# Optimization experiments

Hardware: AMD Instinct MI355X
Metric: run time of the kernel (lower is better)

The kernel has to match this reference:

```python
import jax, jax.numpy as jnp
import numpy as np

HEADS = 16

def _split_qkv(qkv, h):
    # faithful to rearrange 'b t (d k h) -> k b h t d' with k=3
    b, t, e3 = qkv.shape
    d = e3 // (3 * h)
    qkv = qkv.reshape(b, t, d, 3, h)          # (b,t,d,k,h), d-major packing
    qkv = jnp.transpose(qkv, (3, 0, 4, 1, 2))  # (k,b,h,t,d)
    return qkv[0], qkv[1], qkv[2]

def setup_inputs() -> dict:
    key = jax.random.key(0)
    ks = jax.random.split(key, 5)
    b, t, e = 2, 2048, 1024
    s = e ** -0.5
    return {
        "x": jax.random.normal(ks[0], (b, t, e), jnp.float32),
        "tx": jax.random.normal(ks[1], (b, t, e), jnp.float32),
        "Wqkv": jax.random.normal(ks[2], (3 * e, e), jnp.float32) * s,
        "Wtqkv": jax.random.normal(ks[3], (3 * e, e), jnp.float32) * s,
        "Wout": jax.random.normal(ks[4], (e, e), jnp.float32) * s,
    }

def reference(x, tx, Wqkv, Wtqkv, Wout):
    h = HEADS
    e = x.shape[-1]
    d_head = e // h
    scale = jnp.float32(d_head ** 0.5)  # NOTE: module MULTIPLIES by sqrt(d_head)

    qkv = x @ Wqkv.T     # (b,t,3e)
    tqkv = tx @ Wtqkv.T  # (b,t,3e)
    _q, k, v = _split_qkv(qkv, h)      # each (b,h,t,d)
    tq, _tk, _tv = _split_qkv(tqkv, h)

    energy = jnp.einsum('bhid,bhjd->bhij', tq, k) * scale  # (b,h,t,t)
    attn = jax.nn.softmax(energy, axis=-1)
    out = jnp.einsum('bhij,bhjd->bhid', attn, v)           # (b,h,t,d)
    b, _, t, d = out.shape
    out = jnp.transpose(out, (0, 2, 1, 3)).reshape(b, t, h * d)  # 'b h t d -> b t (h d)'
    return out @ Wout.T
```

## Files before the change

### kernel.cpp

```cpp
#include <hip/hip_runtime.h>

typedef unsigned short u16;
typedef unsigned int u32;
typedef __attribute__((ext_vector_type(8))) short short8;
typedef __attribute__((ext_vector_type(4))) float f32x4;

__device__ inline u16 f32_to_bf16(float f) {
  u32 u = __float_as_uint(f);
  u += 0x7fffu + ((u >> 16) & 1u);
  return (u16)(u >> 16);
}
__device__ inline float bf16_to_f32(u16 s) {
  return __uint_as_float(((u32)s) << 16);
}

#if __has_builtin(__builtin_amdgcn_exp2f)
#define EXP2F(x) __builtin_amdgcn_exp2f(x)
#else
#define EXP2F(x) exp2f(x)
#endif

__device__ inline void dma16(const void* gp, void* lp) {
  __builtin_amdgcn_global_load_lds(
      (const __attribute__((address_space(1))) u32*)gp,
      (__attribute__((address_space(3))) u32*)lp, 16, 0, 0);
}

__device__ inline u32 pack_hi16(u32 a, u32 b) {
  return __builtin_amdgcn_perm(b, a, 0x07060302u);
}
__device__ inline uint4 pack_bf16_8(const uint4 a, const uint4 b) {
  uint4 r;
  r.x = pack_hi16(a.x, a.y);
  r.y = pack_hi16(a.z, a.w);
  r.z = pack_hi16(b.x, b.y);
  r.w = pack_hi16(b.z, b.w);
  return r;
}
__device__ inline void split8(const uint4 a, const uint4 b, uint4& hi, uint4& lo) {
  u32 u[8] = {a.x, a.y, a.z, a.w, b.x, b.y, b.z, b.w};
  u32 l[8];
#pragma unroll
  for (int j = 0; j < 8; ++j)
    l[j] = __float_as_uint(__uint_as_float(u[j]) - __uint_as_float(u[j] & 0xffff0000u));
  hi.x = pack_hi16(u[0], u[1]); hi.y = pack_hi16(u[2], u[3]);
  hi.z = pack_hi16(u[4], u[5]); hi.w = pack_hi16(u[6], u[7]);
  lo.x = pack_hi16(l[0], l[1]); lo.y = pack_hi16(l[2], l[3]);
  lo.z = pack_hi16(l[4], l[5]); lo.w = pack_hi16(l[6], l[7]);
}

__global__ void repack_w(const float* __restrict__ Wqkv, const float* __restrict__ Wtqkv,
                         const float* __restrict__ Wout,
                         u16* __restrict__ Wtq_hi, u16* __restrict__ Wtq_lo,
                         u16* __restrict__ Wk_hi,  u16* __restrict__ Wk_lo,
                         u16* __restrict__ Wv_hi,  u16* __restrict__ Woutb) {
  int r = blockIdx.x;
  int part = r >> 10;
  int rr = r & 1023;
  int h = rr >> 6, d = rr & 63;
  const float* src;
  u16 *dh, *dl = nullptr;
  if (part == 0)      { src = Wtqkv + (size_t)(d * 48 + h) * 1024;      dh = Wtq_hi + (size_t)rr * 1024; dl = Wtq_lo + (size_t)rr * 1024; }
  else if (part == 1) { src = Wqkv  + (size_t)(d * 48 + 16 + h) * 1024; dh = Wk_hi  + (size_t)rr * 1024; dl = Wk_lo  + (size_t)rr * 1024; }
  else if (part == 2) { src = Wqkv  + (size_t)(d * 48 + 32 + h) * 1024; dh = Wv_hi  + (size_t)rr * 1024; }
  else                { src = Wout  + (size_t)rr * 1024;                dh = Woutb  + (size_t)rr * 1024; }
  int c = threadIdx.x * 4;
  f32x4 v = *(const f32x4*)&src[c];
  u32 hv[4], lv[4];
#pragma unroll
  for (int j = 0; j < 4; ++j) {
    u16 hb = f32_to_bf16(v[j]);
    hv[j] = hb;
    lv[j] = f32_to_bf16(v[j] - bf16_to_f32(hb));
  }
  uint2 ho; ho.x = hv[0] | (hv[1] << 16); ho.y = hv[2] | (hv[3] << 16);
  *(uint2*)&dh[c] = ho;
  if (dl) {
    uint2 lo; lo.x = lv[0] | (lv[1] << 16); lo.y = lv[2] | (lv[3] << 16);
    *(uint2*)&dl[c] = lo;
  }
}

__global__ __launch_bounds__(256) __attribute__((amdgpu_waves_per_eu(2)))
void proj_fused(const float* __restrict__ x, const float* __restrict__ tx,
                const u16* __restrict__ Wtq_hi, const u16* __restrict__ Wtq_lo,
                const u16* __restrict__ Wk_hi,  const u16* __restrict__ Wk_lo,
                const u16* __restrict__ Wv_hi,
                u16* __restrict__ Qhi, u16* __restrict__ Qlo,
                u16* __restrict__ Khi, u16* __restrict__ Klo,
                u16* __restrict__ Vt, float qscale) {
  __shared__ __align__(16) float Fs[2][128][32];
  __shared__ __align__(16) u16   Hs[2][128][32];
  __shared__ __align__(16) u16   Ls[2][128][32];
  const int tid = threadIdx.x;
  const int wid = tid >> 6, lane = tid & 63;
  const int g = lane >> 4, l16 = lane & 15;
  const int job = blockIdx.y;
  const int tile = blockIdx.x;
  const int wm = (wid & 1) * 64, wn = (wid >> 1) * 64;

  int m0, n0, N, frow0, hrow0;
  const float* Fsrc;
  const u16 *Hsrc;
  const u16 *Lsrc = nullptr;
  if (job == 0) {
    m0 = (tile >> 3) * 128; n0 = (tile & 7) * 128; N = 1024;
    Fsrc = tx; frow0 = m0; Hsrc = Wtq_hi; Lsrc = Wtq_lo; hrow0 = n0;
  } else if (job == 1) {
    m0 = (tile >> 3) * 128; n0 = (tile & 7) * 128; N = 1024;
    Fsrc = x; frow0 = m0; Hsrc = Wk_hi; Lsrc = Wk_lo; hrow0 = n0;
  } else {
    m0 = (tile >> 5) * 128; n0 = (tile & 31) * 128; N = 4096;
    Fsrc = x; frow0 = n0; Hsrc = Wv_hi; hrow0 = m0;
  }

  const int lrow8 = lane >> 3;
  const int gf = (lane & 7) ^ lrow8;
  const int lrow4 = lane >> 2;
  const int gh = (lane & 3) ^ ((lrow4 ^ (lrow4 >> 2)) & 3);

  auto issue_chunk = [&](int k0, int p) {
#pragma unroll
    for (int t = 0; t < 4; ++t) {
      int rb = wid * 32 + t * 8;
      dma16(&Fsrc[(size_t)(frow0 + rb + lrow8) * 1024 + k0 + gf * 4], &Fs[p][rb][0]);
    }
#pragma unroll
    for (int t = 0; t < 2; ++t) {
      int rb = wid * 32 + t * 16;
      size_t ro = (size_t)(hrow0 + rb + lrow4) * 1024 + k0 + gh * 8;
      dma16(&Hsrc[ro], &Hs[p][rb][0]);
      if (job != 2) dma16(&Lsrc[ro], &Ls[p][rb][0]);
    }
  };

  f32x4 acc[4][4];
  const f32x4 zero4 = {0.f, 0.f, 0.f, 0.f};
#pragma unroll
  for (int i = 0; i < 4; ++i)
#pragma unroll
    for (int j = 0; j < 4; ++j) acc[i][j] = zero4;

  const int sw8 = l16 & 7;
  const int sw4 = (l16 ^ (l16 >> 2)) & 3;

  issue_chunk(0, 0);

  for (int k0 = 0; k0 < 1024; k0 += 32) {
    const int p = (k0 >> 5) & 1;
    __syncthreads();
    if (k0 + 32 < 1024) issue_chunk(k0 + 32, p ^ 1);

    if (job != 2) {
      short8 ah[4], al[4], bh4[4], bl4[4];
#pragma unroll
      for (int mi = 0; mi < 4; ++mi) {
        const int R = wm + mi * 16 + l16;
        uint4 u0 = *(const uint4*)&Fs[p][R][((2 * g) ^ sw8) * 4];
        uint4 u1 = *(const uint4*)&Fs[p][R][((2 * g + 1) ^ sw8) * 4];
        uint4 hi, lo;
        split8(u0, u1, hi, lo);
        ah[mi] = *(short8*)&hi;
        al[mi] = *(short8*)&lo;
      }
#pragma unroll
      for (int ni = 0; ni < 4; ++ni) {
        const int R = wn + ni * 16 + l16;
        const int col = (g ^ sw4) * 8;
        bh4[ni] = *(const short8*)&Hs[p][R][col];
        bl4[ni] = *(const short8*)&Ls[p][R][col];
      }
#pragma unroll
      for (int mi = 0; mi < 4; ++mi)
#pragma unroll
        for (int ni = 0; ni < 4; ++ni) {
          acc[mi][ni] = __builtin_amdgcn_mfma_f32_16x16x32_bf16(ah[mi], bh4[ni], acc[mi][ni], 0, 0, 0);
          acc[mi][ni] = __builtin_amdgcn_mfma_f32_16x16x32_bf16(ah[mi], bl4[ni], acc[mi][ni], 0, 0, 0);
          acc[mi][ni] = __builtin_amdgcn_mfma_f32_16x16x32_bf16(al[mi], bh4[ni], acc[mi][ni], 0, 0, 0);
        }
    } else {
      short8 av[4], bx[4];
#pragma unroll
      for (int mi = 0; mi < 4; ++mi)
        av[mi] = *(const short8*)&Hs[p][wm + mi * 16 + l16][(g ^ sw4) * 8];
#pragma unroll
      for (int ni = 0; ni < 4; ++ni) {
        const int R = wn + ni * 16 + l16;
        uint4 u0 = *(const uint4*)&Fs[p][R][((2 * g) ^ sw8) * 4];
        uint4 u1 = *(const uint4*)&Fs[p][R][((2 * g + 1) ^ sw8) * 4];
        uint4 t = pack_bf16_8(u0, u1);
        bx[ni] = *(short8*)&t;
      }
#pragma unroll
      for (int mi = 0; mi < 4; ++mi)
#pragma unroll
        for (int ni = 0; ni < 4; ++ni)
          acc[mi][ni] = __builtin_amdgcn_mfma_f32_16x16x32_bf16(av[mi], bx[ni], acc[mi][ni], 0, 0, 0);
    }
  }

  u16* Chi = (job == 0) ? Qhi : ((job == 1) ? Khi : Vt);
  u16* Clo = (job == 0) ? Qlo : Klo;
  float scale = (job == 0) ? qscale : 1.0f;
#pragma unroll
  for (int mi = 0; mi < 4; ++mi)
#pragma unroll
    for (int ni = 0; ni < 4; ++ni) {
      int row = m0 + wm + mi * 16 + g * 4;
      int col = n0 + wn + ni * 16 + l16;
#pragma unroll
      for (int r = 0; r < 4; ++r) {
        float v = acc[mi][ni][r] * scale;
        size_t o = (size_t)(row + r) * N + col;
        u32 uv = __float_as_uint(v);
        if (job != 2) {
          Chi[o] = (u16)(uv >> 16);
          float lo = v - __uint_as_float(uv & 0xffff0000u);
          Clo[o] = (u16)(__float_as_uint(lo) >> 16);
        } else {
          Chi[o] = (u16)(uv >> 16);
        }
      }
    }
}

__global__ __launch_bounds__(256) __attribute__((amdgpu_waves_per_eu(2, 4)))
void gemm_out(const u16* __restrict__ A, const u16* __restrict__ B,
              float* __restrict__ C, int M, int N, int K) {
  __shared__ __align__(16) u16 As[128][40];
  __shared__ __align__(16) u16 Bs[64][40];
  const int tid = threadIdx.x;
  const int wid = tid >> 6, lane = tid & 63;
  const int g = lane >> 4, l16 = lane & 15;
  const int m0 = blockIdx.y * 128, n0 = blockIdx.x * 64;
  const int wm = (wid & 1) * 64, wn = (wid >> 1) * 32;

  f32x4 acc[4][2];
  const f32x4 zero4 = {0.f, 0.f, 0.f, 0.f};
#pragma unroll
  for (int i = 0; i < 4; ++i)
#pragma unroll
    for (int j = 0; j < 2; ++j) acc[i][j] = zero4;

  uint4 pa[2], pb;
  const int rowA0 = tid >> 2, colA = (tid & 3) * 8;
  const int rowA1 = rowA0 + 64;
  const int rowB = tid >> 2, colB = (tid & 3) * 8;
  pa[0] = *(const uint4*)&A[(size_t)(m0 + rowA0) * K + colA];
  pa[1] = *(const uint4*)&A[(size_t)(m0 + rowA1) * K + colA];
  pb    = *(const uint4*)&B[(size_t)(n0 + rowB) * K + colB];

  for (int k0 = 0; k0 < K; k0 += 32) {
    __syncthreads();
    *(uint4*)&As[rowA0][colA] = pa[0];
    *(uint4*)&As[rowA1][colA] = pa[1];
    *(uint4*)&Bs[rowB][colB] = pb;
    __syncthreads();
    if (k0 + 32 < K) {
      pa[0] = *(const uint4*)&A[(size_t)(m0 + rowA0) * K + k0 + 32 + colA];
      pa[1] = *(const uint4*)&A[(size_t)(m0 + rowA1) * K + k0 + 32 + colA];
      pb    = *(const uint4*)&B[(size_t)(n0 + rowB) * K + k0 + 32 + colB];
    }
    short8 af[4], bfr[2];
#pragma unroll
    for (int mi = 0; mi < 4; ++mi)
      af[mi] = *(const short8*)&As[wm + mi * 16 + l16][g * 8];
#pragma unroll
    for (int ni = 0; ni < 2; ++ni)
      bfr[ni] = *(const short8*)&Bs[wn + ni * 16 + l16][g * 8];
#pragma unroll
    for (int mi = 0; mi < 4; ++mi)
#pragma unroll
      for (int ni = 0; ni < 2; ++ni)
        acc[mi][ni] = __builtin_amdgcn_mfma_f32_16x16x32_bf16(af[mi], bfr[ni], acc[mi][ni], 0, 0, 0);
  }
#pragma unroll
  for (int mi = 0; mi < 4; ++mi)
#pragma unroll
    for (int ni = 0; ni < 2; ++ni) {
      int row = m0 + wm + mi * 16 + g * 4;
      int col = n0 + wn + ni * 16 + l16;
#pragma unroll
      for (int r = 0; r < 4; ++r)
        C[(size_t)(row + r) * N + col] = acc[mi][ni][r];
    }
}

__global__ __launch_bounds__(256)
void attn_fwd(const u16* __restrict__ Qhi, const u16* __restrict__ Qlo,
              const u16* __restrict__ Khi, const u16* __restrict__ Klo,
              const u16* __restrict__ Vt, u16* __restrict__ O) {
  const int blk = blockIdx.x;
  const int qb = blk & 15, bh = blk >> 4;
  const int h = bh & 15, b = bh >> 4;
  const int t0 = qb * 128;
  const int tid = threadIdx.x, wid = tid >> 6, lane = tid & 63;
  const int g = lane >> 4, l16 = lane & 15;
  const int par = g & 1;
  const int hi2 = g >> 1;

  __shared__ __align__(16) u16 Ksh[2][64][64];
  __shared__ __align__(16) u16 Ksl[2][64][64];
  __shared__ __align__(16) u16 Vs[2][64][64];

  const int lrow = lane >> 3;
  const int lgc  = (lane & 7) ^ lrow;
  const size_t kbase = (size_t)(b * 2048) * 1024 + h * 64;
  const size_t vbase = (size_t)(h * 64) * 4096 + b * 2048;

  auto issue_chunk = [&](int j0, int p) {
#pragma unroll
    for (int t = 0; t < 2; ++t) {
      int rbase = wid * 16 + t * 8;
      int row = rbase + lrow;
      dma16(&Khi[kbase + (size_t)(j0 + row) * 1024 + lgc * 8], &Ksh[p][rbase][0]);
      dma16(&Klo[kbase + (size_t)(j0 + row) * 1024 + lgc * 8], &Ksl[p][rbase][0]);
      dma16(&Vt[vbase + (size_t)row * 4096 + j0 + lgc * 8],    &Vs[p][rbase][0]);
    }
  };

  short8 qh[2][2], ql[2][2];
#pragma unroll
  for (int mt = 0; mt < 2; ++mt)
#pragma unroll
    for (int ks = 0; ks < 2; ++ks) {
      size_t qo = (size_t)(b * 2048 + t0 + wid * 32 + mt * 16 + l16) * 1024
                  + h * 64 + ks * 32 + g * 8;
      qh[mt][ks] = *(const short8*)&Qhi[qo];
      ql[mt][ks] = *(const short8*)&Qlo[qo];
    }

  float mrow[2] = {-1.0e30f, -1.0e30f};
  const f32x4 zero4 = {0.f, 0.f, 0.f, 0.f};
  f32x4 acc[2][5];
#pragma unroll
  for (int mt = 0; mt < 2; ++mt)
#pragma unroll
    for (int dn = 0; dn < 5; ++dn) acc[mt][dn] = zero4;

  short8 ones8;
#pragma unroll
  for (int j = 0; j < 8; ++j) ones8[j] = (short)0x3f80;

  union PB { u32 w[4]; short8 v; };

  issue_chunk(0, 0);

  for (int i = 0; i < 32; ++i) {
    const int p = i & 1;
    __syncthreads();
    if (i < 31) issue_chunk((i + 1) * 64, 1 - p);

    f32x4 s[2][4];
#pragma unroll
    for (int mt = 0; mt < 2; ++mt)
#pragma unroll
      for (int n = 0; n < 4; ++n) s[mt][n] = zero4;
#pragma unroll
    for (int ks = 0; ks < 2; ++ks)
#pragma unroll
      for (int n = 0; n < 4; ++n) {
        int col = (((ks * 4 + g) ^ (l16 & 7))) * 8;
        short8 kh = *(const short8*)&Ksh[p][n * 16 + l16][col];
        short8 kl = *(const short8*)&Ksl[p][n * 16 + l16][col];
        s[0][n] = __builtin_amdgcn_mfma_f32_16x16x32_bf16(kh, qh[0][ks], s[0][n], 0, 0, 0);
        s[1][n] = __builtin_amdgcn_mfma_f32_16x16x32_bf16(kh, qh[1][ks], s[1][n], 0, 0, 0);
        s[0][n] = __builtin_amdgcn_mfma_f32_16x16x32_bf16(kh, ql[0][ks], s[0][n], 0, 0, 0);
        s[1][n] = __builtin_amdgcn_mfma_f32_16x16x32_bf16(kh, ql[1][ks], s[1][n], 0, 0, 0);
        s[0][n] = __builtin_amdgcn_mfma_f32_16x16x32_bf16(kl, qh[0][ks], s[0][n], 0, 0, 0);
        s[1][n] = __builtin_amdgcn_mfma_f32_16x16x32_bf16(kl, qh[1][ks], s[1][n], 0, 0, 0);
      }

    PB pb[2][2];
#pragma unroll
    for (int mt = 0; mt < 2; ++mt) {
      float cm = -1.0e30f;
#pragma unroll
      for (int n = 0; n < 4; ++n)
#pragma unroll
        for (int r = 0; r < 4; ++r) cm = fmaxf(cm, s[mt][n][r]);
      cm = fmaxf(cm, __shfl_xor(cm, 16));
      cm = fmaxf(cm, __shfl_xor(cm, 32));
      float mnew = fmaxf(mrow[mt], cm);
      float al = EXP2F(mrow[mt] - mnew);
      mrow[mt] = mnew;
#pragma unroll
      for (int dn = 0; dn < 5; ++dn)
#pragma unroll
        for (int r = 0; r < 4; ++r) acc[mt][dn][r] *= al;

      u32 pk[4][2];
#pragma unroll
      for (int n = 0; n < 4; ++n) {
        float p0 = EXP2F(s[mt][n][0] - mnew);
        float p1 = EXP2F(s[mt][n][1] - mnew);
        float p2 = EXP2F(s[mt][n][2] - mnew);
        float p3 = EXP2F(s[mt][n][3] - mnew);
        pk[n][0] = pack_hi16(__float_as_uint(p0), __float_as_uint(p1));
        pk[n][1] = pack_hi16(__float_as_uint(p2), __float_as_uint(p3));
      }
#pragma unroll
      for (int ks2 = 0; ks2 < 2; ++ks2)
#pragma unroll
        for (int t = 0; t < 4; ++t) {
          int src = (((par << 1) | (t >> 1)) << 4) | l16;
          u32 w0 = (u32)__shfl((int)pk[2 * ks2][t & 1], src);
          u32 w1 = (u32)__shfl((int)pk[2 * ks2 + 1][t & 1], src);
          pb[mt][ks2].w[t] = hi2 ? w1 : w0;
        }
    }

#pragma unroll
    for (int ks2 = 0; ks2 < 2; ++ks2) {
#pragma unroll
      for (int dn = 0; dn < 4; ++dn) {
        int col = (((ks2 * 4 + g) ^ (l16 & 7))) * 8;
        short8 vb = *(const short8*)&Vs[p][dn * 16 + l16][col];
        acc[0][dn] = __builtin_amdgcn_mfma_f32_16x16x32_bf16(vb, pb[0][ks2].v, acc[0][dn], 0, 0, 0);
        acc[1][dn] = __builtin_amdgcn_mfma_f32_16x16x32_bf16(vb, pb[1][ks2].v, acc[1][dn], 0, 0, 0);
      }
      acc[0][4] = __builtin_amdgcn_mfma_f32_16x16x32_bf16(ones8, pb[0][ks2].v, acc[0][4], 0, 0, 0);
      acc[1][4] = __builtin_amdgcn_mfma_f32_16x16x32_bf16(ones8, pb[1][ks2].v, acc[1][4], 0, 0, 0);
    }
  }

#pragma unroll
  for (int mt = 0; mt < 2; ++mt) {
    float inv = 1.f / acc[mt][4][0];
    int qrow = t0 + wid * 32 + mt * 16 + l16;
    size_t base = (size_t)(b * 2048 + qrow) * 1024 + h * 64;
#pragma unroll
    for (int dn = 0; dn < 4; ++dn) {
      u32 o0 = pack_hi16(__float_as_uint(acc[mt][dn][0] * inv),
                         __float_as_uint(acc[mt][dn][1] * inv));
      u32 o1 = pack_hi16(__float_as_uint(acc[mt][dn][2] * inv),
                         __float_as_uint(acc[mt][dn][3] * inv));
      uint2 ov; ov.x = o0; ov.y = o1;
      *(uint2*)&O[base + dn * 16 + g * 4] = ov;
    }
  }
}

extern "C" void kernel_launch(void* const* d_in, const int* in_sizes, int n_in,
                              void* d_out, int out_size, void* d_ws, size_t ws_size,
                              hipStream_t stream) {
  const float* x     = (const float*)d_in[0];
  const float* tx    = (const float*)d_in[1];
  const float* Wqkv  = (const float*)d_in[2];
  const float* Wtqkv = (const float*)d_in[3];
  const float* Wout  = (const float*)d_in[4];
  float* out = (float*)d_out;

  char* ws = (char*)d_ws;
  const size_t MB = 1048576;
  u16* Wtq_hi = (u16*)(ws + 0 * MB);
  u16* Wtq_lo = (u16*)(ws + 2 * MB);
  u16* Wk_hi  = (u16*)(ws + 4 * MB);
  u16* Wk_lo  = (u16*)(ws + 6 * MB);
  u16* Wv_hi  = (u16*)(ws + 8 * MB);
  u16* Woutb  = (u16*)(ws + 10 * MB);
  u16* Qhi    = (u16*)(ws + 12 * MB);
  u16* Qlo    = (u16*)(ws + 20 * MB);
  u16* Khi    = (u16*)(ws + 28 * MB);
  u16* Klo    = (u16*)(ws + 36 * MB);
  u16* Vt     = (u16*)(ws + 44 * MB);
  u16* Ob     = (u16*)(ws + 0 * MB);
  if (ws_size < 52 * MB) return;

  const float QSCALE = 8.0f * 1.4426950408889634f;

  repack_w<<<4096, 256, 0, stream>>>(Wqkv, Wtqkv, Wout,
                                     Wtq_hi, Wtq_lo, Wk_hi, Wk_lo, Wv_hi, Woutb);
  proj_fused<<<dim3(256, 3), 256, 0, stream>>>(x, tx, Wtq_hi, Wtq_lo, Wk_hi, Wk_lo,
                                               Wv_hi, Qhi, Qlo, Khi, Klo, Vt, QSCALE);
  attn_fwd<<<512, 256, 0, stream>>>(Qhi, Qlo, Khi, Klo, Vt, Ob);
  gemm_out<<<dim3(16, 32), 256, 0, stream>>>(Ob, Woutb, out, 4096, 1024, 1024);
}
```

Measured before the change: 316.8 us.

## Use 8 waves per attention block and skip rescaling when max grows little

```diff
diff --git a/kernel.cpp b/kernel.cpp
--- a/kernel.cpp
+++ b/kernel.cpp
@@ -286,7 +286,7 @@
     }
 }
 
-__global__ __launch_bounds__(256)
+__global__ __launch_bounds__(512)
 void attn_fwd(const u16* __restrict__ Qhi, const u16* __restrict__ Qlo,
               const u16* __restrict__ Khi, const u16* __restrict__ Klo,
               const u16* __restrict__ Vt, u16* __restrict__ O) {
@@ -309,34 +309,26 @@
   const size_t vbase = (size_t)(h * 64) * 4096 + b * 2048;
 
   auto issue_chunk = [&](int j0, int p) {
-#pragma unroll
-    for (int t = 0; t < 2; ++t) {
-      int rbase = wid * 16 + t * 8;
-      int row = rbase + lrow;
-      dma16(&Khi[kbase + (size_t)(j0 + row) * 1024 + lgc * 8], &Ksh[p][rbase][0]);
-      dma16(&Klo[kbase + (size_t)(j0 + row) * 1024 + lgc * 8], &Ksl[p][rbase][0]);
-      dma16(&Vt[vbase + (size_t)row * 4096 + j0 + lgc * 8],    &Vs[p][rbase][0]);
-    }
+    const int row = wid * 8 + lrow;
+    dma16(&Khi[kbase + (size_t)(j0 + row) * 1024 + lgc * 8], &Ksh[p][wid * 8][0]);
+    dma16(&Klo[kbase + (size_t)(j0 + row) * 1024 + lgc * 8], &Ksl[p][wid * 8][0]);
+    dma16(&Vt[vbase + (size_t)row * 4096 + j0 + lgc * 8],    &Vs[p][wid * 8][0]);
   };
 
-  short8 qh[2][2], ql[2][2];
-#pragma unroll
-  for (int mt = 0; mt < 2; ++mt)
-#pragma unroll
-    for (int ks = 0; ks < 2; ++ks) {
-      size_t qo = (size_t)(b * 2048 + t0 + wid * 32 + mt * 16 + l16) * 1024
-                  + h * 64 + ks * 32 + g * 8;
-      qh[mt][ks] = *(const short8*)&Qhi[qo];
-      ql[mt][ks] = *(const short8*)&Qlo[qo];
-    }
-
-  float mrow[2] = {-1.0e30f, -1.0e30f};
+  short8 qh[2], ql[2];
+#pragma unroll
+  for (int ks = 0; ks < 2; ++ks) {
+    size_t qo = (size_t)(b * 2048 + t0 + wid * 16 + l16) * 1024
+                + h * 64 + ks * 32 + g * 8;
+    qh[ks] = *(const short8*)&Qhi[qo];
+    ql[ks] = *(const short8*)&Qlo[qo];
+  }
+
+  float mrow = -1.0e30f;
   const f32x4 zero4 = {0.f, 0.f, 0.f, 0.f};
-  f32x4 acc[2][5];
-#pragma unroll
-  for (int mt = 0; mt < 2; ++mt)
-#pragma unroll
-    for (int dn = 0; dn < 5; ++dn) acc[mt][dn] = zero4;
+  f32x4 acc[5];
+#pragma unroll
+  for (int dn = 0; dn < 5; ++dn) acc[dn] = zero4;
 
   short8 ones8;
 #pragma unroll
@@ -351,11 +343,9 @@
     __syncthreads();
     if (i < 31) issue_chunk((i + 1) * 64, 1 - p);
 
-    f32x4 s[2][4];
-#pragma unroll
-    for (int mt = 0; mt < 2; ++mt)
-#pragma unroll
-      for (int n = 0; n < 4; ++n) s[mt][n] = zero4;
+    f32x4 s[4];
+#pragma unroll
+    for (int n = 0; n < 4; ++n) s[n] = zero4;
 #pragma unroll
     for (int ks = 0; ks < 2; ++ks)
 #pragma unroll
@@ -363,52 +353,48 @@
         int col = (((ks * 4 + g) ^ (l16 & 7))) * 8;
         short8 kh = *(const short8*)&Ksh[p][n * 16 + l16][col];
         short8 kl = *(const short8*)&Ksl[p][n * 16 + l16][col];
-        s[0][n] = __builtin_amdgcn_mfma_f32_16x16x32_bf16(kh, qh[0][ks], s[0][n], 0, 0, 0);
-        s[1][n] = __builtin_amdgcn_mfma_f32_16x16x32_bf16(kh, qh[1][ks], s[1][n], 0, 0, 0);
-        s[0][n] = __builtin_amdgcn_mfma_f32_16x16x32_bf16(kh, ql[0][ks], s[0][n], 0, 0, 0);
-        s[1][n] = __builtin_amdgcn_mfma_f32_16x16x32_bf16(kh, ql[1][ks], s[1][n], 0, 0, 0);
-        s[0][n] = __builtin_amdgcn_mfma_f32_16x16x32_bf16(kl, qh[0][ks], s[0][n], 0, 0, 0);
-        s[1][n] = __builtin_amdgcn_mfma_f32_16x16x32_bf16(kl, qh[1][ks], s[1][n], 0, 0, 0);
-      }
-
-    PB pb[2][2];
-#pragma unroll
-    for (int mt = 0; mt < 2; ++mt) {
-      float cm = -1.0e30f;
-#pragma unroll
-      for (int n = 0; n < 4; ++n)
-#pragma unroll
-        for (int r = 0; r < 4; ++r) cm = fmaxf(cm, s[mt][n][r]);
-      cm = fmaxf(cm, __shfl_xor(cm, 16));
-      cm = fmaxf(cm, __shfl_xor(cm, 32));
-      float mnew = fmaxf(mrow[mt], cm);
-      float al = EXP2F(mrow[mt] - mnew);
-      mrow[mt] = mnew;
+        s[n] = __builtin_amdgcn_mfma_f32_16x16x32_bf16(kh, qh[ks], s[n], 0, 0, 0);
+        s[n] = __builtin_amdgcn_mfma_f32_16x16x32_bf16(kh, ql[ks], s[n], 0, 0, 0);
+        s[n] = __builtin_amdgcn_mfma_f32_16x16x32_bf16(kl, qh[ks], s[n], 0, 0, 0);
+      }
+
+    float cm = -1.0e30f;
+#pragma unroll
+    for (int n = 0; n < 4; ++n)
+#pragma unroll
+      for (int r = 0; r < 4; ++r) cm = fmaxf(cm, s[n][r]);
+    cm = fmaxf(cm, __shfl_xor(cm, 16));
+    cm = fmaxf(cm, __shfl_xor(cm, 32));
+    if (!__all(cm <= mrow + 8.0f)) {
+      float mnew = fmaxf(mrow, cm);
+      float al = EXP2F(mrow - mnew);
+      mrow = mnew;
 #pragma unroll
       for (int dn = 0; dn < 5; ++dn)
 #pragma unroll
-        for (int r = 0; r < 4; ++r) acc[mt][dn][r] *= al;
-
-      u32 pk[4][2];
-#pragma unroll
-      for (int n = 0; n < 4; ++n) {
-        float p0 = EXP2F(s[mt][n][0] - mnew);
-        float p1 = EXP2F(s[mt][n][1] - mnew);
-        float p2 = EXP2F(s[mt][n][2] - mnew);
-        float p3 = EXP2F(s[mt][n][3] - mnew);
-        pk[n][0] = pack_hi16(__float_as_uint(p0), __float_as_uint(p1));
-        pk[n][1] = pack_hi16(__float_as_uint(p2), __float_as_uint(p3));
-      }
-#pragma unroll
-      for (int ks2 = 0; ks2 < 2; ++ks2)
-#pragma unroll
-        for (int t = 0; t < 4; ++t) {
-          int src = (((par << 1) | (t >> 1)) << 4) | l16;
-          u32 w0 = (u32)__shfl((int)pk[2 * ks2][t & 1], src);
-          u32 w1 = (u32)__shfl((int)pk[2 * ks2 + 1][t & 1], src);
-          pb[mt][ks2].w[t] = hi2 ? w1 : w0;
-        }
-    }
+        for (int r = 0; r < 4; ++r) acc[dn][r] *= al;
+    }
+
+    u32 pk[4][2];
+#pragma unroll
+    for (int n = 0; n < 4; ++n) {
+      float p0 = EXP2F(s[n][0] - mrow);
+      float p1 = EXP2F(s[n][1] - mrow);
+      float p2 = EXP2F(s[n][2] - mrow);
+      float p3 = EXP2F(s[n][3] - mrow);
+      pk[n][0] = pack_hi16(__float_as_uint(p0), __float_as_uint(p1));
+      pk[n][1] = pack_hi16(__float_as_uint(p2), __float_as_uint(p3));
+    }
+    PB pb[2];
+#pragma unroll
+    for (int ks2 = 0; ks2 < 2; ++ks2)
+#pragma unroll
+      for (int t = 0; t < 4; ++t) {
+        int src = (((par << 1) | (t >> 1)) << 4) | l16;
+        u32 w0 = (u32)__shfl((int)pk[2 * ks2][t & 1], src);
+        u32 w1 = (u32)__shfl((int)pk[2 * ks2 + 1][t & 1], src);
+        pb[ks2].w[t] = hi2 ? w1 : w0;
+      }
 
 #pragma unroll
     for (int ks2 = 0; ks2 < 2; ++ks2) {
@@ -416,28 +402,23 @@
       for (int dn = 0; dn < 4; ++dn) {
         int col = (((ks2 * 4 + g) ^ (l16 & 7))) * 8;
         short8 vb = *(const short8*)&Vs[p][dn * 16 + l16][col];
-        acc[0][dn] = __builtin_amdgcn_mfma_f32_16x16x32_bf16(vb, pb[0][ks2].v, acc[0][dn], 0, 0, 0);
-        acc[1][dn] = __builtin_amdgcn_mfma_f32_16x16x32_bf16(vb, pb[1][ks2].v, acc[1][dn], 0, 0, 0);
-      }
-      acc[0][4] = __builtin_amdgcn_mfma_f32_16x16x32_bf16(ones8, pb[0][ks2].v, acc[0][4], 0, 0, 0);
-      acc[1][4] = __builtin_amdgcn_mfma_f32_16x16x32_bf16(ones8, pb[1][ks2].v, acc[1][4], 0, 0, 0);
-    }
-  }
-
-#pragma unroll
-  for (int mt = 0; mt < 2; ++mt) {
-    float inv = 1.f / acc[mt][4][0];
-    int qrow = t0 + wid * 32 + mt * 16 + l16;
-    size_t base = (size_t)(b * 2048 + qrow) * 1024 + h * 64;
-#pragma unroll
-    for (int dn = 0; dn < 4; ++dn) {
-      u32 o0 = pack_hi16(__float_as_uint(acc[mt][dn][0] * inv),
-                         __float_as_uint(acc[mt][dn][1] * inv));
-      u32 o1 = pack_hi16(__float_as_uint(acc[mt][dn][2] * inv),
-                         __float_as_uint(acc[mt][dn][3] * inv));
-      uint2 ov; ov.x = o0; ov.y = o1;
-      *(uint2*)&O[base + dn * 16 + g * 4] = ov;
-    }
+        acc[dn] = __builtin_amdgcn_mfma_f32_16x16x32_bf16(vb, pb[ks2].v, acc[dn], 0, 0, 0);
+      }
+      acc[4] = __builtin_amdgcn_mfma_f32_16x16x32_bf16(ones8, pb[ks2].v, acc[4], 0, 0, 0);
+    }
+  }
+
+  float inv = 1.f / acc[4][0];
+  int qrow = t0 + wid * 16 + l16;
+  size_t base = (size_t)(b * 2048 + qrow) * 1024 + h * 64;
+#pragma unroll
+  for (int dn = 0; dn < 4; ++dn) {
+    u32 o0 = pack_hi16(__float_as_uint(acc[dn][0] * inv),
+                       __float_as_uint(acc[dn][1] * inv));
+    u32 o1 = pack_hi16(__float_as_uint(acc[dn][2] * inv),
+                       __float_as_uint(acc[dn][3] * inv));
+    uint2 ov; ov.x = o0; ov.y = o1;
+    *(uint2*)&O[base + dn * 16 + g * 4] = ov;
   }
 }
 
@@ -473,6 +454,6 @@
                                      Wtq_hi, Wtq_lo, Wk_hi, Wk_lo, Wv_hi, Woutb);
   proj_fused<<<dim3(256, 3), 256, 0, stream>>>(x, tx, Wtq_hi, Wtq_lo, Wk_hi, Wk_lo,
                                                Wv_hi, Qhi, Qlo, Khi, Klo, Vt, QSCALE);
-  attn_fwd<<<512, 256, 0, stream>>>(Qhi, Qlo, Khi, Klo, Vt, Ob);
+  attn_fwd<<<512, 512, 0, stream>>>(Qhi, Qlo, Khi, Klo, Vt, Ob);
   gemm_out<<<dim3(16, 32), 256, 0, stream>>>(Ob, Woutb, out, 4096, 1024, 1024);
 }
```

After: 304.7 us. -3.8%, faster.
